# Kernel tuning notes

Measured on AMD Instinct MI355X. Metric: run time of the kernel, lower is better.

Reference implementation:

```python
import jax, jax.numpy as jnp
import numpy as np

B, D, N, L, M = 32, 64, 128, 192, 32  # batch, channels, nodes, seq_len, modes
LH = L // 2 + 1  # rfft length = 97


def setup_inputs() -> dict:
    key = jax.random.key(0)
    k1, k2, k3 = jax.random.split(key, 3)
    scale = 1.0 / (D * D)  # 1/(in_channels*out_channels)
    q = jax.random.normal(k1, (B, D, N, L), dtype=jnp.float32)
    w_real = scale * jax.random.uniform(k2, (N, D, D, M), dtype=jnp.float32)
    w_imag = scale * jax.random.uniform(k3, (N, D, D, M), dtype=jnp.float32)
    return {"q": q, "w_real": w_real, "w_imag": w_imag}


def reference(q, w_real, w_imag):
    # mode_select_method='lowest' -> index = [0, 1, ..., M-1] (static)
    index = np.arange(M)
    x = jnp.transpose(q, (0, 2, 1, 3))            # [B, N, D, L]
    x_ft = jnp.fft.rfft(x, axis=-1)               # [B, N, D, LH] complex64
    w = (w_real + 1j * w_imag).astype(jnp.complex64)  # [N, D, D, M]
    sel = x_ft[..., index]                        # gather selected modes [B, N, D, M]
    # fused replacement of the per-mode einsum loop: one batched complex einsum
    out_sel = jnp.einsum('bnim,niom->bnom', sel, w)  # [B, N, D, M]
    out_ft = jnp.zeros((B, N, D, LH), dtype=jnp.complex64).at[..., :M].set(out_sel)
    out = jnp.fft.irfft(out_ft, n=L, axis=-1)     # [B, N, D, L] real
    return jnp.transpose(out, (0, 2, 1, 3))       # [B, D, N, L]
```

## Files before the change

### kernel.cpp

```cpp
#include <hip/hip_runtime.h>
#include <stdint.h>


typedef __attribute__((ext_vector_type(8))) short short8;
typedef __attribute__((ext_vector_type(4))) float f32x4;
typedef __attribute__((ext_vector_type(4))) unsigned short u16x4;

__device__ __forceinline__ unsigned short f2bf(float f) {
  union { float fv; uint32_t u; } v; v.fv = f;
  uint32_t u = v.u;
  u += 0x7fffu + ((u >> 16) & 1u);
  return (unsigned short)(u >> 16);
}

__device__ __forceinline__ f32x4 zero4() { f32x4 z; z[0]=0.f; z[1]=0.f; z[2]=0.f; z[3]=0.f; return z; }

#define TWO_PI_OVER_L (6.283185307179586f / 192.0f)

__global__ __launch_bounds__(512, 2)
void k1_dft(const float* __restrict__ q, unsigned short* __restrict__ Xp) {
  extern __shared__ char smem[];
  const int t = threadIdx.x, lane = t & 63, w = t >> 6;
  const int n = blockIdx.x >> 1, ih = blockIdx.x & 1;

  unsigned short* qb = (unsigned short*)smem;
  char* Fb = smem + 65536;

  for (int idx = t; idx < 64 * 192; idx += 512) {
    int cat = idx / 192, l = idx - cat * 192;
    int m = cat >> 1;
    int r = (m * l) % 192;
    float ang = (float)r * TWO_PI_OVER_L;
    float v = (cat & 1) ? -__sinf(ang) : __cosf(ang);
    *(unsigned short*)(Fb + cat * 400 + l * 2) = f2bf(v);
  }

  f32x4 acc[8][4];
#pragma unroll
  for (int a = 0; a < 8; ++a)
#pragma unroll
    for (int bq = 0; bq < 4; ++bq) acc[a][bq] = zero4();

  for (int kc = 0; kc < 6; ++kc) {
#pragma unroll
    for (int j = 0; j < 16; ++j) {
      int f = j * 512 + t;
      int lg = f & 7, b = (f >> 3) & 31, il = f >> 8;
      const float4 v = *(const float4*)(q + (((b * 64 + ih * 32 + il) * 128 + n) * 192 + kc * 32 + lg * 4));
      u16x4 h; h[0] = f2bf(v.x); h[1] = f2bf(v.y); h[2] = f2bf(v.z); h[3] = f2bf(v.w);
      *(u16x4*)(qb + (il * 32 + b) * 32 + lg * 4) = h;
    }
    __syncthreads();

    short8 Bf[4];
#pragma unroll
    for (int nt = 0; nt < 4; ++nt) {
      int cat = nt * 16 + (lane & 15);
      Bf[nt] = *(const short8*)(Fb + cat * 400 + (kc * 32 + (lane >> 4) * 8) * 2);
    }
#pragma unroll
    for (int mt = 0; mt < 8; ++mt) {
      int Mt = w * 8 + mt;
      int il = Mt >> 1;
      int b = (Mt & 1) * 16 + (lane & 15);
      short8 A = *(const short8*)((const char*)qb + ((il * 32 + b) * 32 + (lane >> 4) * 8) * 2);
#pragma unroll
      for (int nt = 0; nt < 4; ++nt)
        acc[mt][nt] = __builtin_amdgcn_mfma_f32_16x16x32_bf16(A, Bf[nt], acc[mt][nt], 0, 0, 0);
    }
    __syncthreads();
  }

#pragma unroll
  for (int mt = 0; mt < 8; ++mt) {
    int Mt = w * 8 + mt;
    int il = Mt >> 1;
    int b0 = (Mt & 1) * 16 + (lane >> 4) * 4;
#pragma unroll
    for (int nt = 0; nt < 4; ++nt) {
      int cat = nt * 16 + (lane & 15);
      char* base = smem + cat * 2320 + il * 2;
      f32x4 v = acc[mt][nt];
#pragma unroll
      for (int r = 0; r < 4; ++r)
        *(unsigned short*)(base + (b0 + r) * 72) = f2bf(v[r]);
    }
  }
  __syncthreads();

  const int nbase = n * 131072;
#pragma unroll
  for (int j = 0; j < 16; ++j) {
    int f = j * 512 + t;
    int l2 = f & 63, Mt2 = (f >> 6) & 1, c = (f >> 7) & 1, m = f >> 8;
    int cat = 2 * m + c;
    int b = Mt2 * 16 + (l2 & 15);
    int i0 = (l2 >> 4) * 8;
    const char* base = smem + cat * 2320 + b * 72 + i0 * 2;
    u16x4 lo = *(const u16x4*)(base);
    u16x4 hi = *(const u16x4*)(base + 8);
    short8 vv;
    vv[0] = (short)lo[0]; vv[1] = (short)lo[1]; vv[2] = (short)lo[2]; vv[3] = (short)lo[3];
    vv[4] = (short)hi[0]; vv[5] = (short)hi[1]; vv[6] = (short)hi[2]; vv[7] = (short)hi[3];
    int off = nbase + ((((m * 2 + c) * 2 + ih) * 2 + Mt2) * 64 + l2) * 8;
    *(short8*)(Xp + off) = vv;
  }
}

__global__ __launch_bounds__(256, 4)
void k0_repack(const float* __restrict__ wr, const float* __restrict__ wi,
               unsigned short* __restrict__ Wp) {
  __shared__ unsigned short T[32 * 16 * 36];
  const int t = threadIdx.x;
  const int bid = blockIdx.x;
  const int ic = bid & 1, nt = (bid >> 1) & 3, c = (bid >> 3) & 1, n = bid >> 4;
  const float* src = (c ? wi : wr) + ((n * 64 + ic * 32) * 64 + nt * 16) * 32;

#pragma unroll
  for (int j = 0; j < 16; ++j) {
    int f = j * 256 + t;
    int mg = f & 7, o = (f >> 3) & 15, i = f >> 7;
    float4 v = *(const float4*)(src + i * 2048 + o * 32 + mg * 4);
    u16x4 h; h[0] = f2bf(v.x); h[1] = f2bf(v.y); h[2] = f2bf(v.z); h[3] = f2bf(v.w);
    *(u16x4*)(T + (i * 16 + o) * 36 + mg * 4) = h;
  }
  __syncthreads();

  unsigned short* dst = Wp + ((((n * 32) * 2 + c) * 4 + nt) * 2 + ic) * 512;
#pragma unroll
  for (int j = 0; j < 8; ++j) {
    int f = j * 256 + t;
    int m = f >> 6, lidx = f & 63;
    int il0 = (lidx >> 4) * 8, ol = lidx & 15;
    short8 v;
#pragma unroll
    for (int e = 0; e < 8; ++e)
      v[e] = (short)T[((il0 + e) * 16 + ol) * 36 + m];
    *(short8*)(dst + m * 8192 + lidx * 8) = v;
  }
}

__global__ __launch_bounds__(256, 4)
void k2_mix(const unsigned short* __restrict__ Wp, const unsigned short* __restrict__ Xp,
            unsigned short* __restrict__ Yp) {
  __shared__ unsigned short Yl[32 * 132];
  const int t = threadIdx.x, lane = t & 63, w = t >> 6;
  const int n = blockIdx.x >> 5, m = blockIdx.x & 31;

  const unsigned short* xb = Xp + n * 131072 + m * 4096 + lane * 8;
  short8 Ar[2][2], Ai[2][2];
#pragma unroll
  for (int ic = 0; ic < 2; ++ic)
#pragma unroll
    for (int Mt = 0; Mt < 2; ++Mt) {
      Ar[ic][Mt] = *(const short8*)(xb + (ic * 2 + Mt) * 512);
      Ai[ic][Mt] = *(const short8*)(xb + 2048 + (ic * 2 + Mt) * 512);
    }

  const unsigned short* wb = Wp + (n * 32 + m) * 8192 + w * 1024 + lane * 8;
  short8 Br[2], Bi[2], nBi[2];
#pragma unroll
  for (int ic = 0; ic < 2; ++ic) {
    Br[ic] = *(const short8*)(wb + ic * 512);
    Bi[ic] = *(const short8*)(wb + 4096 + ic * 512);
#pragma unroll
    for (int e = 0; e < 8; ++e) nBi[ic][e] = Bi[ic][e] ^ (short)0x8000;
  }

  f32x4 acc[2][2];
#pragma unroll
  for (int a = 0; a < 2; ++a)
#pragma unroll
    for (int b2 = 0; b2 < 2; ++b2) acc[a][b2] = zero4();

#pragma unroll
  for (int ic = 0; ic < 2; ++ic)
#pragma unroll
    for (int Mt = 0; Mt < 2; ++Mt) {
      acc[0][Mt] = __builtin_amdgcn_mfma_f32_16x16x32_bf16(Ar[ic][Mt], Br[ic],  acc[0][Mt], 0, 0, 0);
      acc[0][Mt] = __builtin_amdgcn_mfma_f32_16x16x32_bf16(Ai[ic][Mt], nBi[ic], acc[0][Mt], 0, 0, 0);
      acc[1][Mt] = __builtin_amdgcn_mfma_f32_16x16x32_bf16(Ar[ic][Mt], Bi[ic],  acc[1][Mt], 0, 0, 0);
      acc[1][Mt] = __builtin_amdgcn_mfma_f32_16x16x32_bf16(Ai[ic][Mt], Br[ic],  acc[1][Mt], 0, 0, 0);
    }

  const int ol = lane & 15, g = lane >> 4;
#pragma unroll
  for (int cc = 0; cc < 2; ++cc)
#pragma unroll
    for (int Mt = 0; Mt < 2; ++Mt) {
      f32x4 v = acc[cc][Mt];
#pragma unroll
      for (int r = 0; r < 4; ++r) {
        int b = Mt * 16 + g * 4 + r;
        Yl[b * 132 + cc * 64 + w * 16 + ol] = f2bf(v[r]);
      }
    }
  __syncthreads();

  unsigned short* yb = Yp + n * 131072 + m * 128;
#pragma unroll
  for (int j = 0; j < 2; ++j) {
    int f = j * 256 + t;
    int b = f >> 4, rem = f & 15;
    const unsigned short* p = Yl + b * 132 + rem * 8;
    u16x4 lo = *(const u16x4*)(p);
    u16x4 hi = *(const u16x4*)(p + 4);
    short8 v;
    v[0] = (short)lo[0]; v[1] = (short)lo[1]; v[2] = (short)lo[2]; v[3] = (short)lo[3];
    v[4] = (short)hi[0]; v[5] = (short)hi[1]; v[6] = (short)hi[2]; v[7] = (short)hi[3];
    *(short8*)(yb + b * 4096 + rem * 8) = v;
  }
}

__global__ __launch_bounds__(256, 4)
void k3_idft(const unsigned short* __restrict__ Yp, float* __restrict__ out) {
  extern __shared__ char smem[];
  unsigned short* Yl = (unsigned short*)smem;
  float* ol = (float*)(smem + 8192);
  const int t = threadIdx.x, lane = t & 63, w = t >> 6;
  const int n = blockIdx.x & 127, b = blockIdx.x >> 7;

  const unsigned short* ysrc = Yp + (n * 32 + b) * 4096;
#pragma unroll
  for (int j = 0; j < 2; ++j) {
    int f = j * 256 + t;
    *(short8*)(Yl + f * 8) = *(const short8*)(ysrc + f * 8);
  }

  short8 Af[3][2];
#pragma unroll
  for (int jm = 0; jm < 3; ++jm) {
    int Mt = w + 4 * jm;
    int lt = Mt * 16 + (lane & 15);
#pragma unroll
    for (int kc = 0; kc < 2; ++kc) {
#pragma unroll
      for (int e = 0; e < 8; ++e) {
        int cat = kc * 32 + (lane >> 4) * 8 + e;
        int m = cat >> 1;
        int r = (m * lt) % 192;
        float ang = (float)r * TWO_PI_OVER_L;
        float coef = (m == 0) ? (1.0f / 192.0f) : (2.0f / 192.0f);
        float v = ((cat & 1) ? -__sinf(ang) : __cosf(ang)) * coef;
        Af[jm][kc][e] = (short)f2bf(v);
      }
    }
  }
  __syncthreads();

  f32x4 acc[3][4];
#pragma unroll
  for (int a = 0; a < 3; ++a)
#pragma unroll
    for (int bq = 0; bq < 4; ++bq) acc[a][bq] = zero4();

#pragma unroll
  for (int kc = 0; kc < 2; ++kc) {
    short8 Bf[4];
#pragma unroll
    for (int nt = 0; nt < 4; ++nt)
#pragma unroll
      for (int e = 0; e < 8; ++e) {
        int cat = kc * 32 + (lane >> 4) * 8 + e;
        Bf[nt][e] = (short)Yl[cat * 64 + nt * 16 + (lane & 15)];
      }
#pragma unroll
    for (int jm = 0; jm < 3; ++jm)
#pragma unroll
      for (int nt = 0; nt < 4; ++nt)
        acc[jm][nt] = __builtin_amdgcn_mfma_f32_16x16x32_bf16(Af[jm][kc], Bf[nt], acc[jm][nt], 0, 0, 0);
  }

#pragma unroll
  for (int jm = 0; jm < 3; ++jm) {
    int Mt = w + 4 * jm;
    int l0 = Mt * 16 + (lane >> 4) * 4;
#pragma unroll
    for (int nt = 0; nt < 4; ++nt) {
      int o = nt * 16 + (lane & 15);
      int lp = l0 ^ ((o & 7) << 2);
      *(f32x4*)(ol + o * 192 + lp) = acc[jm][nt];
    }
  }
  __syncthreads();

  float* dst = out + (b * 64 * 128 + n) * 192;
#pragma unroll
  for (int j = 0; j < 12; ++j) {
    int f = j * 256 + t;
    int o = f / 48, g = f - o * 48;
    int lp = g * 4;
    int l = lp ^ ((o & 7) << 2);
    f32x4 v = *(const f32x4*)(ol + o * 192 + lp);
    *(f32x4*)(dst + o * (128 * 192) + l) = v;
  }
}

extern "C" void kernel_launch(void* const* d_in, const int* in_sizes, int n_in,
                              void* d_out, int out_size, void* d_ws, size_t ws_size,
                              hipStream_t stream) {
  const float* q  = (const float*)d_in[0];
  const float* wr = (const float*)d_in[1];
  const float* wi = (const float*)d_in[2];
  float* out = (float*)d_out;

  unsigned short* Xp = (unsigned short*)d_ws;
  unsigned short* Yp = Xp + 16777216;
  unsigned short* Wp = Xp + 33554432;

  hipFuncSetAttribute((const void*)k1_dft,  hipFuncAttributeMaxDynamicSharedMemorySize, 148480);
  hipFuncSetAttribute((const void*)k3_idft, hipFuncAttributeMaxDynamicSharedMemorySize, 57344);

  k1_dft<<<dim3(256), dim3(512), 148480, stream>>>(q, Xp);
  k0_repack<<<dim3(2048), dim3(256), 0, stream>>>(wr, wi, Wp);
  k2_mix<<<dim3(4096), dim3(256), 0, stream>>>(Wp, Xp, Yp);
  k3_idft<<<dim3(4096), dim3(256), 57344, stream>>>(Yp, out);
}
```

Baseline: 194.8 us.

## Restructure forward DFT kernel with per-node double-buffered contiguous q loads

The forward DFT kernel now assigns each block 4 nodes × 4 batches × 32 channels and walks the nodes with a register-staged, double-buffered shared-memory pipeline. Each load reads whole contiguous 192-float rows instead of 32-float chunks. The intent is to overlap global reads with MFMA work and raise the grid from 256 to 512 blocks so more of the GPU is busy. In exchange there are more barriers per node and more stage registers, occupancy is lowered to one block per CU, and the DFT basis table is rebuilt in every block, now twice as many blocks.

```diff
diff --git a/kernel.cpp b/kernel.cpp
--- a/kernel.cpp
+++ b/kernel.cpp
@@ -17,14 +17,40 @@
 
 #define TWO_PI_OVER_L (6.283185307179586f / 192.0f)
 
-__global__ __launch_bounds__(512, 2)
-void k1_dft(const float* __restrict__ q, unsigned short* __restrict__ Xp) {
+__global__ __launch_bounds__(512, 1)
+void k1d_dft(const float* __restrict__ q, unsigned short* __restrict__ Xp) {
   extern __shared__ char smem[];
+  unsigned short* qB0 = (unsigned short*)smem;
+  unsigned short* qB1 = (unsigned short*)(smem + 51200);
+  unsigned short* Fb  = (unsigned short*)(smem + 102400);
+  unsigned short* XE  = (unsigned short*)(smem + 128000);
   const int t = threadIdx.x, lane = t & 63, w = t >> 6;
-  const int n = blockIdx.x >> 1, ih = blockIdx.x & 1;
-
-  unsigned short* qb = (unsigned short*)smem;
-  char* Fb = smem + 65536;
+  const int l15 = lane & 15, g = lane >> 4;
+  const int bid = blockIdx.x;
+  const int ih = bid & 1, bq = (bid >> 1) & 7, nq = bid >> 4;
+  const int b0 = bq * 4;
+
+  int srow[12], sqd[12];
+#pragma unroll
+  for (int j = 0; j < 12; ++j) {
+    int fq = (w * 12 + j) * 64 + lane;
+    srow[j] = fq / 48;
+    sqd[j] = fq - srow[j] * 48;
+  }
+  size_t qoff[12];
+#pragma unroll
+  for (int j = 0; j < 12; ++j) {
+    int row = srow[j];
+    int b = b0 + (row >> 5), i = ih * 32 + (row & 31);
+    qoff[j] = ((size_t)((b * 64 + i) * 128)) * 192 + sqd[j] * 4;
+  }
+  float4 stg[12];
+  {
+    const int n0 = nq * 4;
+#pragma unroll
+    for (int j = 0; j < 12; ++j)
+      stg[j] = *(const float4*)(q + qoff[j] + (size_t)n0 * 192);
+  }
 
   for (int idx = t; idx < 64 * 192; idx += 512) {
     int cat = idx / 192, l = idx - cat * 192;
@@ -32,78 +58,72 @@
     int r = (m * l) % 192;
     float ang = (float)r * TWO_PI_OVER_L;
     float v = (cat & 1) ? -__sinf(ang) : __cosf(ang);
-    *(unsigned short*)(Fb + cat * 400 + l * 2) = f2bf(v);
-  }
-
-  f32x4 acc[8][4];
-#pragma unroll
-  for (int a = 0; a < 8; ++a)
-#pragma unroll
-    for (int bq = 0; bq < 4; ++bq) acc[a][bq] = zero4();
-
-  for (int kc = 0; kc < 6; ++kc) {
-#pragma unroll
-    for (int j = 0; j < 16; ++j) {
-      int f = j * 512 + t;
-      int lg = f & 7, b = (f >> 3) & 31, il = f >> 8;
-      const float4 v = *(const float4*)(q + (((b * 64 + ih * 32 + il) * 128 + n) * 192 + kc * 32 + lg * 4));
-      u16x4 h; h[0] = f2bf(v.x); h[1] = f2bf(v.y); h[2] = f2bf(v.z); h[3] = f2bf(v.w);
-      *(u16x4*)(qb + (il * 32 + b) * 32 + lg * 4) = h;
+    Fb[cat * 200 + l] = f2bf(v);
+  }
+
+#pragma unroll
+  for (int j = 0; j < 12; ++j) {
+    u16x4 h; h[0] = f2bf(stg[j].x); h[1] = f2bf(stg[j].y);
+    h[2] = f2bf(stg[j].z); h[3] = f2bf(stg[j].w);
+    *(u16x4*)(qB0 + srow[j] * 200 + sqd[j] * 4) = h;
+  }
+  __syncthreads();
+
+  for (int nn = 0; nn < 4; ++nn) {
+    const int n = nq * 4 + nn;
+    unsigned short* cur = (nn & 1) ? qB1 : qB0;
+    unsigned short* nxt = (nn & 1) ? qB0 : qB1;
+
+    if (nn < 3) {
+#pragma unroll
+      for (int j = 0; j < 12; ++j)
+        stg[j] = *(const float4*)(q + qoff[j] + (size_t)(n + 1) * 192);
+    }
+
+    f32x4 acc[4];
+#pragma unroll
+    for (int a = 0; a < 4; ++a) acc[a] = zero4();
+    const int row = w * 16 + l15;
+#pragma unroll
+    for (int kc = 0; kc < 6; ++kc) {
+      short8 A = *(const short8*)(cur + row * 200 + kc * 32 + g * 8);
+#pragma unroll
+      for (int nt = 0; nt < 4; ++nt) {
+        short8 Bf = *(const short8*)(Fb + (nt * 16 + l15) * 200 + kc * 32 + g * 8);
+        acc[nt] = __builtin_amdgcn_mfma_f32_16x16x32_bf16(A, Bf, acc[nt], 0, 0, 0);
+      }
+    }
+
+    if (nn < 3) {
+#pragma unroll
+      for (int j = 0; j < 12; ++j) {
+        u16x4 h; h[0] = f2bf(stg[j].x); h[1] = f2bf(stg[j].y);
+        h[2] = f2bf(stg[j].z); h[3] = f2bf(stg[j].w);
+        *(u16x4*)(nxt + srow[j] * 200 + sqd[j] * 4) = h;
+      }
     }
     __syncthreads();
 
-    short8 Bf[4];
+    const int b_loc = w >> 1, i_base = (w & 1) * 16 + g * 4;
 #pragma unroll
     for (int nt = 0; nt < 4; ++nt) {
-      int cat = nt * 16 + (lane & 15);
-      Bf[nt] = *(const short8*)(Fb + cat * 400 + (kc * 32 + (lane >> 4) * 8) * 2);
-    }
-#pragma unroll
-    for (int mt = 0; mt < 8; ++mt) {
-      int Mt = w * 8 + mt;
-      int il = Mt >> 1;
-      int b = (Mt & 1) * 16 + (lane & 15);
-      short8 A = *(const short8*)((const char*)qb + ((il * 32 + b) * 32 + (lane >> 4) * 8) * 2);
-#pragma unroll
-      for (int nt = 0; nt < 4; ++nt)
-        acc[mt][nt] = __builtin_amdgcn_mfma_f32_16x16x32_bf16(A, Bf[nt], acc[mt][nt], 0, 0, 0);
+      int cat = nt * 16 + l15;
+      f32x4 v = acc[nt];
+#pragma unroll
+      for (int r = 0; r < 4; ++r)
+        XE[cat * 132 + b_loc * 32 + i_base + r] = f2bf(v[r]);
     }
     __syncthreads();
-  }
-
-#pragma unroll
-  for (int mt = 0; mt < 8; ++mt) {
-    int Mt = w * 8 + mt;
-    int il = Mt >> 1;
-    int b0 = (Mt & 1) * 16 + (lane >> 4) * 4;
-#pragma unroll
-    for (int nt = 0; nt < 4; ++nt) {
-      int cat = nt * 16 + (lane & 15);
-      char* base = smem + cat * 2320 + il * 2;
-      f32x4 v = acc[mt][nt];
-#pragma unroll
-      for (int r = 0; r < 4; ++r)
-        *(unsigned short*)(base + (b0 + r) * 72) = f2bf(v[r]);
-    }
-  }
-  __syncthreads();
-
-  const int nbase = n * 131072;
-#pragma unroll
-  for (int j = 0; j < 16; ++j) {
-    int f = j * 512 + t;
-    int l2 = f & 63, Mt2 = (f >> 6) & 1, c = (f >> 7) & 1, m = f >> 8;
-    int cat = 2 * m + c;
-    int b = Mt2 * 16 + (l2 & 15);
-    int i0 = (l2 >> 4) * 8;
-    const char* base = smem + cat * 2320 + b * 72 + i0 * 2;
-    u16x4 lo = *(const u16x4*)(base);
-    u16x4 hi = *(const u16x4*)(base + 8);
-    short8 vv;
-    vv[0] = (short)lo[0]; vv[1] = (short)lo[1]; vv[2] = (short)lo[2]; vv[3] = (short)lo[3];
-    vv[4] = (short)hi[0]; vv[5] = (short)hi[1]; vv[6] = (short)hi[2]; vv[7] = (short)hi[3];
-    int off = nbase + ((((m * 2 + c) * 2 + ih) * 2 + Mt2) * 64 + l2) * 8;
-    *(short8*)(Xp + off) = vv;
+
+#pragma unroll
+    for (int cc2 = 0; cc2 < 2; ++cc2) {
+      int ch = cc2 * 512 + t;
+      int m = ch >> 5, c = (ch >> 4) & 1, g2 = (ch >> 2) & 3, dl = ch & 3;
+      short8 v = *(const short8*)(XE + (2 * m + c) * 132 + dl * 32 + g2 * 8);
+      int lanep = g2 * 16 + (b0 & 15) + dl;
+      int off = n * 131072 + ((((m * 2 + c) * 2 + ih) * 2 + (b0 >> 4)) * 64 + lanep) * 8;
+      *(short8*)(Xp + off) = v;
+    }
   }
 }
 
@@ -288,8 +308,8 @@
 #pragma unroll
   for (int j = 0; j < 12; ++j) {
     int f = j * 256 + t;
-    int o = f / 48, g = f - o * 48;
-    int lp = g * 4;
+    int o = f / 48, g2 = f - o * 48;
+    int lp = g2 * 4;
     int l = lp ^ ((o & 7) << 2);
     f32x4 v = *(const f32x4*)(ol + o * 192 + lp);
     *(f32x4*)(dst + o * (128 * 192) + l) = v;
@@ -308,10 +328,10 @@
   unsigned short* Yp = Xp + 16777216;
   unsigned short* Wp = Xp + 33554432;
 
-  hipFuncSetAttribute((const void*)k1_dft,  hipFuncAttributeMaxDynamicSharedMemorySize, 148480);
+  hipFuncSetAttribute((const void*)k1d_dft, hipFuncAttributeMaxDynamicSharedMemorySize, 144896);
   hipFuncSetAttribute((const void*)k3_idft, hipFuncAttributeMaxDynamicSharedMemorySize, 57344);
 
-  k1_dft<<<dim3(256), dim3(512), 148480, stream>>>(q, Xp);
+  k1d_dft<<<dim3(512), dim3(512), 144896, stream>>>(q, Xp);
   k0_repack<<<dim3(2048), dim3(256), 0, stream>>>(wr, wi, Wp);
   k2_mix<<<dim3(4096), dim3(256), 0, stream>>>(Wp, Xp, Yp);
   k3_idft<<<dim3(4096), dim3(256), 57344, stream>>>(Yp, out);
```

After: 185.9 us. -4.6%, faster.
